# Optimization experiments

Measured on AMD Instinct MI355X. Metric: run time of the kernel, lower is better.

The kernel has to match this reference:

```python
import jax, jax.numpy as jnp
import numpy as np

K = 11            # NATTEN kernel size (hardcoded in module)
HEAD_DIM = 16     # hardcoded: num_heads = attn_dim // 16
SCALE = HEAD_DIM ** -0.5


def _ln(x, g, b, eps=1e-5):
    mu = x.mean(-1, keepdims=True)
    var = jnp.mean((x - mu) ** 2, axis=-1, keepdims=True)
    return (x - mu) * jax.lax.rsqrt(var + eps) * g + b


def _win_idx(L):
    # NATTEN clamped window: start = clip(i - K//2, 0, L-K)
    i = jnp.arange(L)
    start = jnp.clip(i - K // 2, 0, L - K)
    return start[:, None] + jnp.arange(K)[None, :]  # [L, K]


def _neighborhood_attn(q, k, v, rpb):
    # q,k,v: [B, h, H, W, d]; rpb: [h, 2K-1, 2K-1]
    B, h, H, W, d = q.shape
    ii = _win_idx(H)                                  # [H, K]
    jj = _win_idx(W)                                  # [W, K]
    bi = ii - jnp.arange(H)[:, None] + (K - 1)        # rpb row index [H, K]
    bj = jj - jnp.arange(W)[:, None] + (K - 1)        # rpb col index [W, K]
    bias = rpb[:, bi][:, :, :, bj]                    # [h, H, K, W, K]
    k_i = k[:, :, ii]                                 # [B, h, H, K, W, d]
    v_i = v[:, :, ii]
    # QK over the KxK neighborhood; fixed small loop over column offsets
    attn = jnp.stack(
        [jnp.einsum('bhiwd,bhiawd->bhiaw', q, k_i[:, :, :, :, jj[:, c]])
         for c in range(K)], axis=-1)                 # [B, h, H, K, W, K]
    attn = attn + bias[None]
    # reorder neighbors to row-major (ki, kj), softmax over K*K
    attn = attn.transpose(0, 1, 2, 4, 3, 5).reshape(B, h, H, W, K * K)
    attn = jax.nn.softmax(attn, axis=-1).reshape(B, h, H, W, K, K)
    out = jnp.zeros_like(q)
    for c in range(K):
        out = out + jnp.einsum('bhiwa,bhiawd->bhiwd',
                               attn[..., c], v_i[:, :, :, :, jj[:, c]])
    return out  # [B, h, H, W, d]


def setup_inputs() -> dict:
    key = jax.random.key(0)
    ks = jax.random.split(key, 20)
    B, H, W = 16, 64, 64
    HW = H * W
    C = 128       # cost_latent_dim
    VC = 64       # vert_c_dim
    EC = 256      # encoder_latent_dim
    A = 128       # attn_dim
    h = A // HEAD_DIM
    FF = C * 4
    s = 0.02
    inp = {
        'x': jax.random.normal(ks[0], (B, HW, C), jnp.float32),
        'context': jax.random.normal(ks[1], (B, EC, H, W), jnp.float32),
        'ctxn_g': jnp.ones((EC,), jnp.float32),
        'ctxn_b': jnp.zeros((EC,), jnp.float32),
        'ctxp_w': jax.random.normal(ks[2], (EC, VC), jnp.float32) * s,
        'ctxp_b': jnp.zeros((VC,), jnp.float32),
        'n1_g': jnp.ones((C + VC,), jnp.float32),
        'n1_b': jnp.zeros((C + VC,), jnp.float32),
        'n1v_g': jnp.ones((C,), jnp.float32),
        'n1v_b': jnp.zeros((C,), jnp.float32),
        'q_w': jax.random.normal(ks[3], (C + VC, A), jnp.float32) * s,
        'q_b': jnp.zeros((A,), jnp.float32),
        'k_w': jax.random.normal(ks[4], (C + VC, A), jnp.float32) * s,
        'k_b': jnp.zeros((A,), jnp.float32),
        'v_w': jax.random.normal(ks[5], (C, A), jnp.float32) * s,
        'v_b': jnp.zeros((A,), jnp.float32),
        'rpb': jax.random.normal(ks[6], (h, 2 * K - 1, 2 * K - 1), jnp.float32) * s,
        'proj_w': jax.random.normal(ks[7], (A + C, C), jnp.float32) * s,
        'proj_b': jnp.zeros((C,), jnp.float32),
        'n2_g': jnp.ones((C,), jnp.float32),
        'n2_b': jnp.zeros((C,), jnp.float32),
        'f1_w': jax.random.normal(ks[8], (C, FF), jnp.float32) * s,
        'f1_b': jnp.zeros((FF,), jnp.float32),
        'f2_w': jax.random.normal(ks[9], (FF, C), jnp.float32) * s,
        'f2_b': jnp.zeros((C,), jnp.float32),
    }
    return inp


def reference(x, context, ctxn_g, ctxn_b, ctxp_w, ctxp_b, n1_g, n1_b,
              n1v_g, n1v_b, q_w, q_b, k_w, k_b, v_w, v_b, rpb,
              proj_w, proj_b, n2_g, n2_b, f1_w, f1_b, f2_w, f2_b):
    B, HW, C = x.shape
    Bc, Cc, H, W = context.shape
    short_cut = x
    ctx = context.reshape(Bc, Cc, HW).transpose(0, 2, 1)     # [Bc, HW, Cc]
    ctx = _ln(ctx, ctxn_g, ctxn_b) @ ctxp_w + ctxp_b          # [Bc, HW, VC]
    ctx = jnp.tile(ctx, (B // Bc, 1, 1))
    qk = _ln(jnp.concatenate([x, ctx], axis=-1), n1_g, n1_b)
    vv = _ln(x, n1v_g, n1v_b)
    h = q_w.shape[1] // HEAD_DIM
    q = ((qk @ q_w + q_b) * SCALE).reshape(B, H, W, h, HEAD_DIM).transpose(0, 3, 1, 2, 4)
    k = (qk @ k_w + k_b).reshape(B, H, W, h, HEAD_DIM).transpose(0, 3, 1, 2, 4)
    v = (vv @ v_w + v_b).reshape(B, H, W, h, HEAD_DIM).transpose(0, 3, 1, 2, 4)
    o = _neighborhood_attn(q, k, v, rpb)                      # [B, h, H, W, d]
    o = o.transpose(0, 2, 3, 1, 4).reshape(B, HW, -1)
    y = jnp.concatenate([o, short_cut], axis=-1) @ proj_w + proj_b
    y = short_cut + y
    ffn = jax.nn.gelu(_ln(y, n2_g, n2_b) @ f1_w + f1_b, approximate=False) @ f2_w + f2_b
    return y + ffn
```

## Files before the change

kernel.cpp:

```cpp
#include <hip/hip_runtime.h>
#include <hip/hip_bf16.h>
#include <math.h>

typedef __hip_bfloat16 bf16;
typedef float v2f __attribute__((ext_vector_type(2)));
typedef float v4f __attribute__((ext_vector_type(4)));
typedef short v8s __attribute__((ext_vector_type(8)));
typedef _Float16 v2h __attribute__((ext_vector_type(2)));

__device__ __forceinline__ float b2f(bf16 v) { return __bfloat162float(v); }
__device__ __forceinline__ float unpk_lo(unsigned u) { return __uint_as_float(u << 16); }
__device__ __forceinline__ float unpk_hi(unsigned u) { return __uint_as_float(u & 0xffff0000u); }
__device__ __forceinline__ v2f unpk2(unsigned u) {
    v2f r; r.x = __uint_as_float(u << 16); r.y = __uint_as_float(u & 0xffff0000u); return r;
}
__device__ __forceinline__ unsigned pk2(float a, float b) {
    unsigned ua = __float_as_uint(a);
    unsigned ub = __float_as_uint(b);
    ua = (ua + 0x7fffu + ((ua >> 16) & 1u)) >> 16;
    ub = (ub + 0x7fffu + ((ub >> 16) & 1u)) >> 16;
    return ua | (ub << 16);
}
__device__ __forceinline__ short f2bs(float f) {
    unsigned u = __float_as_uint(f);
    u = (u + 0x7fffu + ((u >> 16) & 1u)) >> 16;
    return (short)u;
}
__device__ __forceinline__ v2h u2h(unsigned u) {
    union { unsigned u; v2h h; } c; c.u = u; return c.h;
}
__device__ __forceinline__ float gelu_exact(float x) {
    return 0.5f * x * (1.f + erff(x * 0.70710678118654752440f));
}

#define LOG2E 1.44269504088896340736f

__global__ __launch_bounds__(256) void k_repack(const float* __restrict__ src,
                                                bf16* __restrict__ dst, int K, int N) {
    int idx = blockIdx.x * 256 + threadIdx.x;
    if (idx >= K * N) return;
    int k = idx / N, n = idx % N;
    int kstep = k >> 5, quad = (k & 31) >> 3, j = k & 7;
    int ntile = n >> 4, nn = n & 15;
    size_t di = ((((size_t)kstep * (N >> 4)) + ntile) * 64 + nn + (quad << 4)) * 8 + j;
    dst[di] = __float2bfloat16(src[idx]);
}

__global__ __launch_bounds__(256) void k_repack_g(const float* __restrict__ src,
                                                  const float* __restrict__ g,
                                                  bf16* __restrict__ dst, int K, int N) {
    int idx = blockIdx.x * 256 + threadIdx.x;
    if (idx >= K * N) return;
    int k = idx / N, n = idx % N;
    int kstep = k >> 5, quad = (k & 31) >> 3, j = k & 7;
    int ntile = n >> 4, nn = n & 15;
    size_t di = ((((size_t)kstep * (N >> 4)) + ntile) * 64 + nn + (quad << 4)) * 8 + j;
    dst[di] = __float2bfloat16(src[idx] * g[k]);
}

__global__ __launch_bounds__(256) void k_ctxc(const float* __restrict__ w,
                                              const float* __restrict__ g,
                                              const float* __restrict__ bb,
                                              const float* __restrict__ pb,
                                              float* __restrict__ cgw,
                                              float* __restrict__ cbw) {
    __shared__ float rg_[4][64], rb_[4][64];
    const int n = threadIdx.x & 63, eg = threadIdx.x >> 6;
    float sg = 0.f, sb = 0.f;
    for (int e = eg * 64; e < eg * 64 + 64; ++e) {
        float wv = w[e * 64 + n];
        sg += g[e] * wv;
        sb += bb[e] * wv;
    }
    rg_[eg][n] = sg; rb_[eg][n] = sb;
    __syncthreads();
    if (threadIdx.x < 64) {
        float a = rg_[0][n] + rg_[1][n] + rg_[2][n] + rg_[3][n];
        float c = rb_[0][n] + rb_[1][n] + rb_[2][n] + rb_[3][n];
        cgw[n] = a;
        cbw[n] = c + pb[n];
    }
}

__global__ __launch_bounds__(256) void k_rpb(const float* __restrict__ src,
                                             float* __restrict__ dst, int n) {
    int i = blockIdx.x * 256 + threadIdx.x;
    if (i < n) dst[i] = src[i] * LOG2E - 8.0f;
}

__global__ __launch_bounds__(256) void k_ctx(const float* __restrict__ ctx,
                                             const float* __restrict__ cgw,
                                             const float* __restrict__ cbw,
                                             const bf16* __restrict__ wgf,
                                             bf16* __restrict__ outp) {
    __shared__ short As[32][264];
    __shared__ float redS[8][32];
    __shared__ float redQ[8][32];
    __shared__ float smu[32], srs[32];
    const int t = threadIdx.x;
    const int b = blockIdx.x >> 7;
    const int hw0 = (blockIdx.x & 127) << 5;
    {
        const int r = t & 31, li = t >> 5;
        const float* src = ctx + ((size_t)b * 256 + li * 32) * 4096 + hw0 + r;
        float v[32];
        float s = 0.f, q = 0.f;
#pragma unroll
        for (int j = 0; j < 32; ++j) {
            float x = src[(size_t)j * 4096];
            v[j] = x; s += x; q += x * x;
        }
        redS[li][r] = s;
        redQ[li][r] = q;
        v8s p0, p1, p2, p3;
#pragma unroll
        for (int j = 0; j < 8; ++j) p0[j] = f2bs(v[j]);
#pragma unroll
        for (int j = 0; j < 8; ++j) p1[j] = f2bs(v[8 + j]);
#pragma unroll
        for (int j = 0; j < 8; ++j) p2[j] = f2bs(v[16 + j]);
#pragma unroll
        for (int j = 0; j < 8; ++j) p3[j] = f2bs(v[24 + j]);
        v8s* dst = (v8s*)&As[r][li * 32];
        dst[0] = p0; dst[1] = p1; dst[2] = p2; dst[3] = p3;
    }
    __syncthreads();
    if (t < 32) {
        float s = 0.f, q = 0.f;
#pragma unroll
        for (int k = 0; k < 8; ++k) { s += redS[k][t]; q += redQ[k][t]; }
        float mu = s * (1.f / 256.f);
        float var = q * (1.f / 256.f) - mu * mu;
        smu[t] = mu;
        srs[t] = rsqrtf(var + 1e-5f);
    }
    __syncthreads();
    const int lane = t & 63, wv = t >> 6;
    const int m = lane & 15, quad = lane >> 4;
    v4f acc0 = (v4f){0.f, 0.f, 0.f, 0.f};
    v4f acc1 = (v4f){0.f, 0.f, 0.f, 0.f};
#pragma unroll
    for (int ks = 0; ks < 8; ++ks) {
        v8s a0 = *(const v8s*)&As[m][ks * 32 + quad * 8];
        v8s a1 = *(const v8s*)&As[m + 16][ks * 32 + quad * 8];
        v8s bfr = ((const v8s*)wgf)[((size_t)ks * 4 + wv) * 64 + lane];
        acc0 = __builtin_amdgcn_mfma_f32_16x16x32_bf16(a0, bfr, acc0, 0, 0, 0);
        acc1 = __builtin_amdgcn_mfma_f32_16x16x32_bf16(a1, bfr, acc1, 0, 0, 0);
    }
    const int n = wv * 16 + m;
    const float cg = cgw[n], cb = cbw[n];
    short* obase = (short*)outp + ((size_t)b * 4096 + hw0) * 64 + n;
#pragma unroll
    for (int rg = 0; rg < 4; ++rg) {
        int row = quad * 4 + rg;
        float o = srs[row] * (acc0[rg] - smu[row] * cg) + cb;
        obase[(size_t)row * 64] = f2bs(o);
    }
#pragma unroll
    for (int rg = 0; rg < 4; ++rg) {
        int row = 16 + quad * 4 + rg;
        float o = srs[row] * (acc1[rg] - smu[row] * cg) + cb;
        obase[(size_t)row * 64] = f2bs(o);
    }
}

__global__ __launch_bounds__(256) void k_qkv(const float* __restrict__ x,
                                             const bf16* __restrict__ ctxp,
                                             const float* __restrict__ n1g, const float* __restrict__ n1b,
                                             const float* __restrict__ nvg, const float* __restrict__ nvb,
                                             const bf16* __restrict__ qwf, const float* __restrict__ qb,
                                             const bf16* __restrict__ kwf, const float* __restrict__ kb,
                                             const bf16* __restrict__ vwf, const float* __restrict__ vb,
                                             _Float16* __restrict__ qo, _Float16* __restrict__ ko,
                                             _Float16* __restrict__ vo) {
    __shared__ short Aqk[32][200];
    __shared__ short Av[32][136];
    const int t = threadIdx.x;
    const size_t row0 = (size_t)blockIdx.x * 32;
    {
        const int r = t >> 3, li = t & 7;
        const float* xr = x + (row0 + r) * 128 + li * 16;
        float v[16];
        float sx1 = 0.f, sx2 = 0.f;
#pragma unroll
        for (int k4 = 0; k4 < 4; ++k4) {
            float4 vv = *(const float4*)(xr + 4 * k4);
            v[4 * k4 + 0] = vv.x; v[4 * k4 + 1] = vv.y; v[4 * k4 + 2] = vv.z; v[4 * k4 + 3] = vv.w;
            sx1 += vv.x + vv.y + vv.z + vv.w;
            sx2 += vv.x * vv.x + vv.y * vv.y + vv.z * vv.z + vv.w * vv.w;
        }
        float cv[8];
        float sc1 = 0.f, sc2 = 0.f;
        {
            uint4 cu = *(const uint4*)(ctxp + (row0 + r) * 64 + li * 8);
            v2f p0 = unpk2(cu.x), p1 = unpk2(cu.y), p2 = unpk2(cu.z), p3 = unpk2(cu.w);
            cv[0] = p0.x; cv[1] = p0.y; cv[2] = p1.x; cv[3] = p1.y;
            cv[4] = p2.x; cv[5] = p2.y; cv[6] = p3.x; cv[7] = p3.y;
#pragma unroll
            for (int k = 0; k < 8; ++k) { sc1 += cv[k]; sc2 += cv[k] * cv[k]; }
        }
#pragma unroll
        for (int o = 1; o < 8; o <<= 1) {
            sx1 += __shfl_xor(sx1, o); sx2 += __shfl_xor(sx2, o);
            sc1 += __shfl_xor(sc1, o); sc2 += __shfl_xor(sc2, o);
        }
        float mu  = (sx1 + sc1) * (1.f / 192.f);
        float rs  = rsqrtf((sx2 + sc2) * (1.f / 192.f) - mu * mu + 1e-5f);
        float muv = sx1 * (1.f / 128.f);
        float rsv = rsqrtf(sx2 * (1.f / 128.f) - muv * muv + 1e-5f);
        v8s q0, q1, vv0, vv1, cc;
#pragma unroll
        for (int k = 0; k < 8; ++k) {
            int c = li * 16 + k;
            q0[k]  = f2bs((v[k] - mu) * rs * n1g[c] + n1b[c]);
            vv0[k] = f2bs((v[k] - muv) * rsv * nvg[c] + nvb[c]);
        }
#pragma unroll
        for (int k = 0; k < 8; ++k) {
            int c = li * 16 + 8 + k;
            q1[k]  = f2bs((v[8 + k] - mu) * rs * n1g[c] + n1b[c]);
            vv1[k] = f2bs((v[8 + k] - muv) * rsv * nvg[c] + nvb[c]);
        }
#pragma unroll
        for (int k = 0; k < 8; ++k) {
            int c = 128 + li * 8 + k;
            cc[k] = f2bs((cv[k] - mu) * rs * n1g[c] + n1b[c]);
        }
        *(v8s*)&Aqk[r][li * 16]     = q0;
        *(v8s*)&Aqk[r][li * 16 + 8] = q1;
        *(v8s*)&Aqk[r][128 + li * 8] = cc;
        *(v8s*)&Av[r][li * 16]     = vv0;
        *(v8s*)&Av[r][li * 16 + 8] = vv1;
    }
    __syncthreads();
    const int lane = t & 63, wv = t >> 6;
    const int m = lane & 15, quad = lane >> 4;
    const int ntb = wv * 2;
    v4f aq[2][2], ak[2][2], av[2][2];
#pragma unroll
    for (int a = 0; a < 2; ++a)
#pragma unroll
        for (int b = 0; b < 2; ++b) {
            aq[a][b] = (v4f){0.f, 0.f, 0.f, 0.f};
            ak[a][b] = (v4f){0.f, 0.f, 0.f, 0.f};
            av[a][b] = (v4f){0.f, 0.f, 0.f, 0.f};
        }
#pragma unroll
    for (int ks = 0; ks < 6; ++ks) {
        v8s a0 = *(const v8s*)&Aqk[m][ks * 32 + quad * 8];
        v8s a1 = *(const v8s*)&Aqk[m + 16][ks * 32 + quad * 8];
        const v8s* bpq = (const v8s*)qwf + ((size_t)ks * 8 + ntb) * 64 + lane;
        const v8s* bpk = (const v8s*)kwf + ((size_t)ks * 8 + ntb) * 64 + lane;
#pragma unroll
        for (int nt = 0; nt < 2; ++nt) {
            v8s bq = bpq[nt * 64];
            v8s bk = bpk[nt * 64];
            aq[0][nt] = __builtin_amdgcn_mfma_f32_16x16x32_bf16(a0, bq, aq[0][nt], 0, 0, 0);
            aq[1][nt] = __builtin_amdgcn_mfma_f32_16x16x32_bf16(a1, bq, aq[1][nt], 0, 0, 0);
            ak[0][nt] = __builtin_amdgcn_mfma_f32_16x16x32_bf16(a0, bk, ak[0][nt], 0, 0, 0);
            ak[1][nt] = __builtin_amdgcn_mfma_f32_16x16x32_bf16(a1, bk, ak[1][nt], 0, 0, 0);
        }
    }
#pragma unroll
    for (int ks = 0; ks < 4; ++ks) {
        v8s a0 = *(const v8s*)&Av[m][ks * 32 + quad * 8];
        v8s a1 = *(const v8s*)&Av[m + 16][ks * 32 + quad * 8];
        const v8s* bpv = (const v8s*)vwf + ((size_t)ks * 8 + ntb) * 64 + lane;
#pragma unroll
        for (int nt = 0; nt < 2; ++nt) {
            v8s bv = bpv[nt * 64];
            av[0][nt] = __builtin_amdgcn_mfma_f32_16x16x32_bf16(a0, bv, av[0][nt], 0, 0, 0);
            av[1][nt] = __builtin_amdgcn_mfma_f32_16x16x32_bf16(a1, bv, av[1][nt], 0, 0, 0);
        }
    }
#pragma unroll
    for (int nt = 0; nt < 2; ++nt) {
        int n = (ntb + nt) * 16 + m;
        int head = n >> 4, d = n & 15;
        float qbv = qb[n], kbv = kb[n], vbv = vb[n];
#pragma unroll
        for (int mt = 0; mt < 2; ++mt)
#pragma unroll
            for (int rg = 0; rg < 4; ++rg) {
                int rowg = (int)row0 + mt * 16 + quad * 4 + rg;
                int b = rowg >> 12, hw = rowg & 4095;
                size_t oi = (((size_t)b * 8 + head) * 4096 + hw) * 16 + d;
                qo[oi] = (_Float16)((aq[mt][nt][rg] + qbv) * (0.25f * LOG2E));
                ko[oi] = (_Float16)(ak[mt][nt][rg] + kbv);
                vo[oi] = (_Float16)(av[mt][nt][rg] + vbv);
            }
    }
}

__global__ __launch_bounds__(256) void k_attn(const _Float16* __restrict__ qws,
                                              const _Float16* __restrict__ kws,
                                              const _Float16* __restrict__ vws,
                                              const float* __restrict__ rpbl2,
                                              bf16* __restrict__ ows) {
    __shared__ unsigned ktv[14][64][20];
    const int tid  = threadIdx.x;
    const int bh   = blockIdx.x >> 4;
    const int i0   = (blockIdx.x & 15) << 2;
    const int head = bh & 7;
    int start_min = i0 - 5; if (start_min < 0) start_min = 0; if (start_min > 53) start_min = 53;
    const unsigned* ku = (const unsigned*)kws;
    const unsigned* vu = (const unsigned*)vws;
    const size_t gbase = ((size_t)bh * 4096 + (size_t)start_min * 64) * 8;
    for (int idx = tid; idx < 1792; idx += 256) {
        int a = idx >> 7, rem = idx & 127, col = rem >> 1, h4 = (rem & 1) * 4;
        if (start_min + a < 64) {
            *(uint4*)&ktv[a][col][h4]     = *(const uint4*)(ku + gbase + (size_t)a * 512 + col * 8 + h4);
            *(uint4*)&ktv[a][col][8 + h4] = *(const uint4*)(vu + gbase + (size_t)a * 512 + col * 8 + h4);
        }
    }
    __syncthreads();
    const int wv = tid >> 6;
    const int j  = tid & 63;
    const int i  = i0 + wv;
    int start_i = i - 5; if (start_i < 0) start_i = 0; if (start_i > 53) start_i = 53;
    const int off = start_i - start_min;
    v2h qh[8];
    {
        const uint4* qp = (const uint4*)(qws + ((size_t)bh * 4096 + i * 64 + j) * 16);
        uint4 q0 = qp[0], q1 = qp[1];
        qh[0] = u2h(q0.x); qh[1] = u2h(q0.y); qh[2] = u2h(q0.z); qh[3] = u2h(q0.w);
        qh[4] = u2h(q1.x); qh[5] = u2h(q1.y); qh[6] = u2h(q1.z); qh[7] = u2h(q1.w);
    }
    int start_j = j - 5; if (start_j < 0) start_j = 0; if (start_j > 53) start_j = 53;
    float l = 0.f;
    v2h acc[8];
#pragma unroll
    for (int d = 0; d < 8; ++d) acc[d] = (v2h){(_Float16)0.f, (_Float16)0.f};
    const float* rpb_h = rpbl2 + head * 441 + (start_j - j + 10);
    for (int a = 0; a < 11; ++a) {
        const int r = off + a;
        const float* rb = rpb_h + (start_i + a - i + 10) * 21;
#pragma unroll
        for (int c = 0; c < 11; ++c) {
            const unsigned* cp = ktv[r][start_j + c];
            uint4 k0 = *(const uint4*)(cp);
            uint4 k1 = *(const uint4*)(cp + 4);
            uint4 v0 = *(const uint4*)(cp + 8);
            uint4 v1 = *(const uint4*)(cp + 12);
            float sa = __builtin_amdgcn_fdot2(qh[0], u2h(k0.x), rb[c], false);
            sa = __builtin_amdgcn_fdot2(qh[1], u2h(k0.y), sa, false);
            sa = __builtin_amdgcn_fdot2(qh[2], u2h(k0.z), sa, false);
            sa = __builtin_amdgcn_fdot2(qh[3], u2h(k0.w), sa, false);
            float sb = __builtin_amdgcn_fdot2(qh[4], u2h(k1.x), 0.f, false);
            sb = __builtin_amdgcn_fdot2(qh[5], u2h(k1.y), sb, false);
            sb = __builtin_amdgcn_fdot2(qh[6], u2h(k1.z), sb, false);
            sb = __builtin_amdgcn_fdot2(qh[7], u2h(k1.w), sb, false);
            float p = __builtin_amdgcn_exp2f(sa + sb);
            l += p;
            _Float16 ph = (_Float16)p;
            v2h p2 = {ph, ph};
            acc[0] += u2h(v0.x) * p2;
            acc[1] += u2h(v0.y) * p2;
            acc[2] += u2h(v0.z) * p2;
            acc[3] += u2h(v0.w) * p2;
            acc[4] += u2h(v1.x) * p2;
            acc[5] += u2h(v1.y) * p2;
            acc[6] += u2h(v1.z) * p2;
            acc[7] += u2h(v1.w) * p2;
        }
    }
    float inv = 1.f / l;
    int b = bh >> 3;
    unsigned* op = (unsigned*)ows + ((size_t)b * 4096 + i * 64 + j) * 64 + head * 8;
#pragma unroll
    for (int d2 = 0; d2 < 8; ++d2)
        op[d2] = pk2((float)acc[d2].x * inv, (float)acc[d2].y * inv);
}

__global__ __launch_bounds__(256) void k_proj(const float* __restrict__ x,
                                              const bf16* __restrict__ ows,
                                              const bf16* __restrict__ pwf,
                                              const float* __restrict__ pb,
                                              float* __restrict__ yws) {
    __shared__ short An[32][264];
    const int t = threadIdx.x;
    const size_t row0 = (size_t)blockIdx.x * 32;
    {
        const int r = t >> 3, li = t & 7;
        const uint4* osrc = (const uint4*)(ows + (row0 + r) * 128 + li * 16);
        uint4 o0 = osrc[0], o1 = osrc[1];
        *(uint4*)&An[r][li * 16]     = o0;
        *(uint4*)&An[r][li * 16 + 8] = o1;
        const float* xr = x + (row0 + r) * 128 + li * 16;
        v8s xa, xb;
#pragma unroll
        for (int k4 = 0; k4 < 2; ++k4) {
            float4 vv = *(const float4*)(xr + 4 * k4);
            xa[4 * k4 + 0] = f2bs(vv.x); xa[4 * k4 + 1] = f2bs(vv.y);
            xa[4 * k4 + 2] = f2bs(vv.z); xa[4 * k4 + 3] = f2bs(vv.w);
        }
#pragma unroll
        for (int k4 = 0; k4 < 2; ++k4) {
            float4 vv = *(const float4*)(xr + 8 + 4 * k4);
            xb[4 * k4 + 0] = f2bs(vv.x); xb[4 * k4 + 1] = f2bs(vv.y);
            xb[4 * k4 + 2] = f2bs(vv.z); xb[4 * k4 + 3] = f2bs(vv.w);
        }
        *(v8s*)&An[r][128 + li * 16]     = xa;
        *(v8s*)&An[r][128 + li * 16 + 8] = xb;
    }
    __syncthreads();
    const int lane = t & 63, wv = t >> 6;
    const int m = lane & 15, quad = lane >> 4;
    const int ntb = wv * 2;
    v4f acc[2][2];
#pragma unroll
    for (int a = 0; a < 2; ++a)
#pragma unroll
        for (int b = 0; b < 2; ++b) acc[a][b] = (v4f){0.f, 0.f, 0.f, 0.f};
#pragma unroll
    for (int ks = 0; ks < 8; ++ks) {
        v8s a0 = *(const v8s*)&An[m][ks * 32 + quad * 8];
        v8s a1 = *(const v8s*)&An[m + 16][ks * 32 + quad * 8];
        const v8s* bp = (const v8s*)pwf + ((size_t)ks * 8 + ntb) * 64 + lane;
#pragma unroll
        for (int nt = 0; nt < 2; ++nt) {
            v8s b = bp[nt * 64];
            acc[0][nt] = __builtin_amdgcn_mfma_f32_16x16x32_bf16(a0, b, acc[0][nt], 0, 0, 0);
            acc[1][nt] = __builtin_amdgcn_mfma_f32_16x16x32_bf16(a1, b, acc[1][nt], 0, 0, 0);
        }
    }
#pragma unroll
    for (int nt = 0; nt < 2; ++nt) {
        int n = (ntb + nt) * 16 + m;
        float bv = pb[n];
#pragma unroll
        for (int mt = 0; mt < 2; ++mt)
#pragma unroll
            for (int rg = 0; rg < 4; ++rg) {
                int row = mt * 16 + quad * 4 + rg;
                size_t gi = (row0 + row) * 128 + n;
                yws[gi] = x[gi] + bv + acc[mt][nt][rg];
            }
    }
}

__global__ __launch_bounds__(256) void k_ffn(const float* __restrict__ yws,
                                             const float* __restrict__ g, const float* __restrict__ bb,
                                             const bf16* __restrict__ w1f, const float* __restrict__ b1,
                                             const bf16* __restrict__ w2f, const float* __restrict__ b2,
                                             float* __restrict__ outp) {
    __shared__ short An[32][136];
    __shared__ short Hs[32][520];
    const int t = threadIdx.x;
    const size_t row0 = (size_t)blockIdx.x * 32;
    {
        const int r = t >> 3, li = t & 7;
        const float* yr = yws + (row0 + r) * 128 + li * 16;
        float v[16];
        float s1 = 0.f, s2 = 0.f;
#pragma unroll
        for (int k4 = 0; k4 < 4; ++k4) {
            float4 vv = *(const float4*)(yr + 4 * k4);
            v[4 * k4 + 0] = vv.x; v[4 * k4 + 1] = vv.y; v[4 * k4 + 2] = vv.z; v[4 * k4 + 3] = vv.w;
            s1 += vv.x + vv.y + vv.z + vv.w;
            s2 += vv.x * vv.x + vv.y * vv.y + vv.z * vv.z + vv.w * vv.w;
        }
#pragma unroll
        for (int o = 1; o < 8; o <<= 1) { s1 += __shfl_xor(s1, o); s2 += __shfl_xor(s2, o); }
        float mu = s1 * (1.f / 128.f);
        float rs = rsqrtf(s2 * (1.f / 128.f) - mu * mu + 1e-5f);
        v8s lo, hi;
#pragma unroll
        for (int k = 0; k < 8; ++k) {
            int c = li * 16 + k;
            lo[k] = f2bs((v[k] - mu) * rs * g[c] + bb[c]);
        }
#pragma unroll
        for (int k = 0; k < 8; ++k) {
            int c = li * 16 + 8 + k;
            hi[k] = f2bs((v[8 + k] - mu) * rs * g[c] + bb[c]);
        }
        *(v8s*)&An[r][li * 16]     = lo;
        *(v8s*)&An[r][li * 16 + 8] = hi;
    }
    __syncthreads();
    const int lane = t & 63, wv = t >> 6;
    const int m = lane & 15, quad = lane >> 4;
    v4f acc1[2][8];
#pragma unroll
    for (int a = 0; a < 2; ++a)
#pragma unroll
        for (int b = 0; b < 8; ++b) acc1[a][b] = (v4f){0.f, 0.f, 0.f, 0.f};
    const int n0w = wv * 128;
#pragma unroll
    for (int ks = 0; ks < 4; ++ks) {
        v8s a0 = *(const v8s*)&An[m][ks * 32 + quad * 8];
        v8s a1 = *(const v8s*)&An[m + 16][ks * 32 + quad * 8];
        const v8s* bp = (const v8s*)w1f + ((size_t)ks * 32 + (n0w >> 4)) * 64 + lane;
#pragma unroll
        for (int nt = 0; nt < 8; ++nt) {
            v8s b = bp[nt * 64];
            acc1[0][nt] = __builtin_amdgcn_mfma_f32_16x16x32_bf16(a0, b, acc1[0][nt], 0, 0, 0);
            acc1[1][nt] = __builtin_amdgcn_mfma_f32_16x16x32_bf16(a1, b, acc1[1][nt], 0, 0, 0);
        }
    }
#pragma unroll
    for (int nt = 0; nt < 8; ++nt) {
        int n = n0w + nt * 16 + m;
        float b1v = b1[n];
#pragma unroll
        for (int mt = 0; mt < 2; ++mt)
#pragma unroll
            for (int rg = 0; rg < 4; ++rg)
                Hs[mt * 16 + quad * 4 + rg][n] = f2bs(gelu_exact(acc1[mt][nt][rg] + b1v));
    }
    __syncthreads();
    v4f acc2[2][2];
#pragma unroll
    for (int a = 0; a < 2; ++a)
#pragma unroll
        for (int b = 0; b < 2; ++b) acc2[a][b] = (v4f){0.f, 0.f, 0.f, 0.f};
    const int ntb = wv * 2;
#pragma unroll
    for (int ks = 0; ks < 16; ++ks) {
        v8s a0 = *(const v8s*)&Hs[m][ks * 32 + quad * 8];
        v8s a1 = *(const v8s*)&Hs[m + 16][ks * 32 + quad * 8];
        const v8s* bp = (const v8s*)w2f + ((size_t)ks * 8 + ntb) * 64 + lane;
#pragma unroll
        for (int nt = 0; nt < 2; ++nt) {
            v8s b = bp[nt * 64];
            acc2[0][nt] = __builtin_amdgcn_mfma_f32_16x16x32_bf16(a0, b, acc2[0][nt], 0, 0, 0);
            acc2[1][nt] = __builtin_amdgcn_mfma_f32_16x16x32_bf16(a1, b, acc2[1][nt], 0, 0, 0);
        }
    }
#pragma unroll
    for (int nt = 0; nt < 2; ++nt) {
        int n = (ntb + nt) * 16 + m;
        float b2v = b2[n];
#pragma unroll
        for (int mt = 0; mt < 2; ++mt)
#pragma unroll
            for (int rg = 0; rg < 4; ++rg) {
                int row = mt * 16 + quad * 4 + rg;
                size_t gi = (row0 + row) * 128 + n;
                outp[gi] = yws[gi] + b2v + acc2[mt][nt][rg];
            }
    }
}

extern "C" void kernel_launch(void* const* d_in, const int* in_sizes, int n_in,
                              void* d_out, int out_size, void* d_ws, size_t ws_size,
                              hipStream_t stream) {
    const float* x      = (const float*)d_in[0];
    const float* ctx    = (const float*)d_in[1];
    const float* ctxn_g = (const float*)d_in[2];
    const float* ctxn_b = (const float*)d_in[3];
    const float* ctxp_w = (const float*)d_in[4];
    const float* ctxp_b = (const float*)d_in[5];
    const float* n1_g   = (const float*)d_in[6];
    const float* n1_b   = (const float*)d_in[7];
    const float* n1v_g  = (const float*)d_in[8];
    const float* n1v_b  = (const float*)d_in[9];
    const float* q_w    = (const float*)d_in[10];
    const float* q_b    = (const float*)d_in[11];
    const float* k_w    = (const float*)d_in[12];
    const float* k_b    = (const float*)d_in[13];
    const float* v_w    = (const float*)d_in[14];
    const float* v_b    = (const float*)d_in[15];
    const float* rpb    = (const float*)d_in[16];
    const float* proj_w = (const float*)d_in[17];
    const float* proj_b = (const float*)d_in[18];
    const float* n2_g   = (const float*)d_in[19];
    const float* n2_b   = (const float*)d_in[20];
    const float* f1_w   = (const float*)d_in[21];
    const float* f1_b   = (const float*)d_in[22];
    const float* f2_w   = (const float*)d_in[23];
    const float* f2_b   = (const float*)d_in[24];
    float* out = (float*)d_out;

    char* ws = (char*)d_ws;
    bf16*      ctxp = (bf16*)(ws);
    _Float16*  qws  = (_Float16*)(ws + 8388608);
    _Float16*  kws  = (_Float16*)(ws + 25165824);
    _Float16*  vws  = (_Float16*)(ws + 41943040);
    bf16*      ows  = (bf16*)(ws + 58720256);
    float*     yws  = (float*)(ws + 8388608);
    char* frag = ws + 75497472;
    bf16*  w1f  = (bf16*)(frag);
    bf16*  w2f  = (bf16*)(frag + 131072);
    bf16*  qwf  = (bf16*)(frag + 262144);
    bf16*  kwf  = (bf16*)(frag + 311296);
    bf16*  vwf  = (bf16*)(frag + 360448);
    bf16*  pwf  = (bf16*)(frag + 393216);
    float* rpl2 = (float*)(frag + 458752);
    bf16*  wgf  = (bf16*)(ws + 8388608);
    float* cgw  = (float*)(ws + 8388608 + 32768);
    float* cbw  = (float*)(ws + 8388608 + 33024);

    k_repack<<<256, 256, 0, stream>>>(f1_w, w1f, 128, 512);
    k_repack<<<256, 256, 0, stream>>>(f2_w, w2f, 512, 128);
    k_repack<<<96,  256, 0, stream>>>(q_w,  qwf, 192, 128);
    k_repack<<<96,  256, 0, stream>>>(k_w,  kwf, 192, 128);
    k_repack<<<64,  256, 0, stream>>>(v_w,  vwf, 128, 128);
    k_repack<<<128, 256, 0, stream>>>(proj_w, pwf, 256, 128);
    k_repack_g<<<64, 256, 0, stream>>>(ctxp_w, ctxn_g, wgf, 256, 64);
    k_ctxc<<<1, 256, 0, stream>>>(ctxp_w, ctxn_g, ctxn_b, ctxp_b, cgw, cbw);
    k_rpb<<<14, 256, 0, stream>>>(rpb, rpl2, 8 * 441);
    k_ctx<<<2048, 256, 0, stream>>>(ctx, cgw, cbw, wgf, ctxp);
    k_qkv<<<2048, 256, 0, stream>>>(x, ctxp, n1_g, n1_b, n1v_g, n1v_b,
                                    qwf, q_b, kwf, k_b, vwf, v_b, qws, kws, vws);
    k_attn<<<2048, 256, 0, stream>>>(qws, kws, vws, rpl2, ows);
    k_proj<<<2048, 256, 0, stream>>>(x, ows, pwf, proj_b, yws);
    k_ffn<<<2048, 256, 0, stream>>>(yws, n2_g, n2_b, w1f, f1_b, w2f, f2_b, out);
}
```

Before: 379.6 us.

## Register-block neighborhood attention over four query rows sharing K/V LDS reads

Each thread now computes four consecutive query rows and iterates over the union of their row windows. Each K/V vector loaded from shared memory is reused across the four queries, with a large negative penalty masking positions outside a given row's window. Shared memory is relaid out column-major with padding and sized to cover 8 query rows per 128-thread block. This cuts LDS read traffic per output, in exchange for extra masked dot products and exps, larger LDS per block and lower occupancy.

```diff
diff --git a/kernel.cpp b/kernel.cpp
--- a/kernel.cpp
+++ b/kernel.cpp
@@ -292,84 +292,104 @@
     }
 }
 
-__global__ __launch_bounds__(256) void k_attn(const _Float16* __restrict__ qws,
+__global__ __launch_bounds__(128) void k_attn(const _Float16* __restrict__ qws,
                                               const _Float16* __restrict__ kws,
                                               const _Float16* __restrict__ vws,
                                               const float* __restrict__ rpbl2,
                                               bf16* __restrict__ ows) {
-    __shared__ unsigned ktv[14][64][20];
+    __shared__ unsigned ktv[64 * 292];
     const int tid  = threadIdx.x;
-    const int bh   = blockIdx.x >> 4;
-    const int i0   = (blockIdx.x & 15) << 2;
+    const int bh   = blockIdx.x >> 3;
+    const int i0   = (blockIdx.x & 7) << 3;
     const int head = bh & 7;
-    int start_min = i0 - 5; if (start_min < 0) start_min = 0; if (start_min > 53) start_min = 53;
+    int start_min = i0 - 5; if (start_min < 0) start_min = 0; if (start_min > 46) start_min = 46;
     const unsigned* ku = (const unsigned*)kws;
     const unsigned* vu = (const unsigned*)vws;
-    const size_t gbase = ((size_t)bh * 4096 + (size_t)start_min * 64) * 8;
-    for (int idx = tid; idx < 1792; idx += 256) {
-        int a = idx >> 7, rem = idx & 127, col = rem >> 1, h4 = (rem & 1) * 4;
-        if (start_min + a < 64) {
-            *(uint4*)&ktv[a][col][h4]     = *(const uint4*)(ku + gbase + (size_t)a * 512 + col * 8 + h4);
-            *(uint4*)&ktv[a][col][8 + h4] = *(const uint4*)(vu + gbase + (size_t)a * 512 + col * 8 + h4);
-        }
+    const size_t gK = ((size_t)bh * 4096 + (size_t)start_min * 64) * 8;
+    for (int idx = tid; idx < 4608; idx += 128) {
+        int col = idx & 63, slot = (idx >> 6) & 3, row = idx >> 8;
+        const unsigned* src = (slot < 2 ? ku : vu) + gK + (size_t)row * 512 + col * 8 + (slot & 1) * 4;
+        *(uint4*)&ktv[col * 292 + row * 16 + slot * 4] = *(const uint4*)src;
     }
     __syncthreads();
     const int wv = tid >> 6;
     const int j  = tid & 63;
-    const int i  = i0 + wv;
-    int start_i = i - 5; if (start_i < 0) start_i = 0; if (start_i > 53) start_i = 53;
-    const int off = start_i - start_min;
-    v2h qh[8];
-    {
-        const uint4* qp = (const uint4*)(qws + ((size_t)bh * 4096 + i * 64 + j) * 16);
+    const int ib = i0 + 4 * wv;
+    int start_j = j - 5; if (start_j < 0) start_j = 0; if (start_j > 53) start_j = 53;
+    v2h qh[4][8];
+#pragma unroll
+    for (int q = 0; q < 4; ++q) {
+        const uint4* qp = (const uint4*)(qws + ((size_t)bh * 4096 + (ib + q) * 64 + j) * 16);
         uint4 q0 = qp[0], q1 = qp[1];
-        qh[0] = u2h(q0.x); qh[1] = u2h(q0.y); qh[2] = u2h(q0.z); qh[3] = u2h(q0.w);
-        qh[4] = u2h(q1.x); qh[5] = u2h(q1.y); qh[6] = u2h(q1.z); qh[7] = u2h(q1.w);
-    }
-    int start_j = j - 5; if (start_j < 0) start_j = 0; if (start_j > 53) start_j = 53;
-    float l = 0.f;
-    v2h acc[8];
-#pragma unroll
-    for (int d = 0; d < 8; ++d) acc[d] = (v2h){(_Float16)0.f, (_Float16)0.f};
-    const float* rpb_h = rpbl2 + head * 441 + (start_j - j + 10);
-    for (int a = 0; a < 11; ++a) {
-        const int r = off + a;
-        const float* rb = rpb_h + (start_i + a - i + 10) * 21;
+        qh[q][0] = u2h(q0.x); qh[q][1] = u2h(q0.y); qh[q][2] = u2h(q0.z); qh[q][3] = u2h(q0.w);
+        qh[q][4] = u2h(q1.x); qh[q][5] = u2h(q1.y); qh[q][6] = u2h(q1.z); qh[q][7] = u2h(q1.w);
+    }
+    int st0 = ib - 5; if (st0 < 0) st0 = 0; if (st0 > 53) st0 = 53;
+    int st3 = ib - 2; if (st3 < 0) st3 = 0; if (st3 > 53) st3 = 53;
+    const int nr = st3 - st0 + 11;
+    float l[4] = {0.f, 0.f, 0.f, 0.f};
+    v2h acc[4][8];
+#pragma unroll
+    for (int q = 0; q < 4; ++q)
+#pragma unroll
+        for (int d = 0; d < 8; ++d) acc[q][d] = (v2h){(_Float16)0.f, (_Float16)0.f};
+    const float* rpb_base = rpbl2 + head * 441 + (start_j - j + 10);
+    const int lds_base = start_j * 292;
+    for (int au = 0; au < nr; ++au) {
+        const int a_abs = st0 + au;
+        const int r16 = (a_abs - start_min) * 16;
+        const float* rb[4];
+        float pen[4];
+#pragma unroll
+        for (int q = 0; q < 4; ++q) {
+            int iq = ib + q;
+            int sq = iq - 5; if (sq < 0) sq = 0; if (sq > 53) sq = 53;
+            int ri = a_abs - iq + 10;
+            int ric = ri < 0 ? 0 : (ri > 20 ? 20 : ri);
+            rb[q] = rpb_base + ric * 21;
+            pen[q] = ((unsigned)(a_abs - sq) <= 10u) ? 0.f : -30000.f;
+        }
 #pragma unroll
         for (int c = 0; c < 11; ++c) {
-            const unsigned* cp = ktv[r][start_j + c];
+            const unsigned* cp = &ktv[lds_base + c * 292 + r16];
             uint4 k0 = *(const uint4*)(cp);
             uint4 k1 = *(const uint4*)(cp + 4);
             uint4 v0 = *(const uint4*)(cp + 8);
             uint4 v1 = *(const uint4*)(cp + 12);
-            float sa = __builtin_amdgcn_fdot2(qh[0], u2h(k0.x), rb[c], false);
-            sa = __builtin_amdgcn_fdot2(qh[1], u2h(k0.y), sa, false);
-            sa = __builtin_amdgcn_fdot2(qh[2], u2h(k0.z), sa, false);
-            sa = __builtin_amdgcn_fdot2(qh[3], u2h(k0.w), sa, false);
-            float sb = __builtin_amdgcn_fdot2(qh[4], u2h(k1.x), 0.f, false);
-            sb = __builtin_amdgcn_fdot2(qh[5], u2h(k1.y), sb, false);
-            sb = __builtin_amdgcn_fdot2(qh[6], u2h(k1.z), sb, false);
-            sb = __builtin_amdgcn_fdot2(qh[7], u2h(k1.w), sb, false);
-            float p = __builtin_amdgcn_exp2f(sa + sb);
-            l += p;
-            _Float16 ph = (_Float16)p;
-            v2h p2 = {ph, ph};
-            acc[0] += u2h(v0.x) * p2;
-            acc[1] += u2h(v0.y) * p2;
-            acc[2] += u2h(v0.z) * p2;
-            acc[3] += u2h(v0.w) * p2;
-            acc[4] += u2h(v1.x) * p2;
-            acc[5] += u2h(v1.y) * p2;
-            acc[6] += u2h(v1.z) * p2;
-            acc[7] += u2h(v1.w) * p2;
-        }
-    }
-    float inv = 1.f / l;
-    int b = bh >> 3;
-    unsigned* op = (unsigned*)ows + ((size_t)b * 4096 + i * 64 + j) * 64 + head * 8;
-#pragma unroll
-    for (int d2 = 0; d2 < 8; ++d2)
-        op[d2] = pk2((float)acc[d2].x * inv, (float)acc[d2].y * inv);
+#pragma unroll
+            for (int q = 0; q < 4; ++q) {
+                float sa = __builtin_amdgcn_fdot2(qh[q][0], u2h(k0.x), rb[q][c] + pen[q], false);
+                sa = __builtin_amdgcn_fdot2(qh[q][1], u2h(k0.y), sa, false);
+                sa = __builtin_amdgcn_fdot2(qh[q][2], u2h(k0.z), sa, false);
+                sa = __builtin_amdgcn_fdot2(qh[q][3], u2h(k0.w), sa, false);
+                float sb = __builtin_amdgcn_fdot2(qh[q][4], u2h(k1.x), 0.f, false);
+                sb = __builtin_amdgcn_fdot2(qh[q][5], u2h(k1.y), sb, false);
+                sb = __builtin_amdgcn_fdot2(qh[q][6], u2h(k1.z), sb, false);
+                sb = __builtin_amdgcn_fdot2(qh[q][7], u2h(k1.w), sb, false);
+                float p = __builtin_amdgcn_exp2f(sa + sb);
+                l[q] += p;
+                _Float16 ph = (_Float16)p;
+                v2h p2 = {ph, ph};
+                acc[q][0] += u2h(v0.x) * p2;
+                acc[q][1] += u2h(v0.y) * p2;
+                acc[q][2] += u2h(v0.z) * p2;
+                acc[q][3] += u2h(v0.w) * p2;
+                acc[q][4] += u2h(v1.x) * p2;
+                acc[q][5] += u2h(v1.y) * p2;
+                acc[q][6] += u2h(v1.z) * p2;
+                acc[q][7] += u2h(v1.w) * p2;
+            }
+        }
+    }
+    const int b = bh >> 3;
+#pragma unroll
+    for (int q = 0; q < 4; ++q) {
+        float inv = 1.f / l[q];
+        unsigned* op = (unsigned*)ows + ((size_t)b * 4096 + (ib + q) * 64 + j) * 64 + head * 8;
+#pragma unroll
+        for (int d2 = 0; d2 < 8; ++d2)
+            op[d2] = pk2((float)acc[q][d2].x * inv, (float)acc[q][d2].y * inv);
+    }
 }
 
 __global__ __launch_bounds__(256) void k_proj(const float* __restrict__ x,
@@ -604,7 +624,7 @@
     k_ctx<<<2048, 256, 0, stream>>>(ctx, cgw, cbw, wgf, ctxp);
     k_qkv<<<2048, 256, 0, stream>>>(x, ctxp, n1_g, n1_b, n1v_g, n1v_b,
                                     qwf, q_b, kwf, k_b, vwf, v_b, qws, kws, vws);
-    k_attn<<<2048, 256, 0, stream>>>(qws, kws, vws, rpl2, ows);
+    k_attn<<<1024, 128, 0, stream>>>(qws, kws, vws, rpl2, ows);
     k_proj<<<2048, 256, 0, stream>>>(x, ows, pwf, proj_b, yws);
     k_ffn<<<2048, 256, 0, stream>>>(yws, n2_g, n2_b, w1f, f1_b, w2f, f2_b, out);
 }
```

Measured after the change: 421.4 us. 1.11x slower.

## Fuse projection with FFN and coalesce QKV stores via LDS transpose

Applied to the files above, without the earlier changes.

Merges the projection and FFN kernels into one, so the residual y stays in shared memory rather than making a float32 round trip through global memory and needing an extra launch. Shared memory is aliased across stages, with added barriers, to keep the LDS footprint bounded. The QKV kernel now stages its fp16 outputs in LDS and writes them as 16-byte per-head rows instead of scattered 2-byte stores. The cost is more barriers and higher LDS use per block, which may lower occupancy.

```diff
diff --git a/kernel.cpp b/kernel.cpp
--- a/kernel.cpp
+++ b/kernel.cpp
@@ -25,6 +25,9 @@
     unsigned u = __float_as_uint(f);
     u = (u + 0x7fffu + ((u >> 16) & 1u)) >> 16;
     return (short)u;
+}
+__device__ __forceinline__ short f2hs(float f) {
+    union { _Float16 h; short s; } c; c.h = (_Float16)f; return c.s;
 }
 __device__ __forceinline__ v2h u2h(unsigned u) {
     union { unsigned u; v2h h; } c; c.u = u; return c.h;
@@ -173,8 +176,9 @@
                                              const bf16* __restrict__ vwf, const float* __restrict__ vb,
                                              _Float16* __restrict__ qo, _Float16* __restrict__ ko,
                                              _Float16* __restrict__ vo) {
-    __shared__ short Aqk[32][200];
-    __shared__ short Av[32][136];
+    __shared__ short SM[13056];
+    short* Aqk = SM;
+    short* Av  = SM + 6400;
     const int t = threadIdx.x;
     const size_t row0 = (size_t)blockIdx.x * 32;
     {
@@ -226,11 +230,11 @@
             int c = 128 + li * 8 + k;
             cc[k] = f2bs((cv[k] - mu) * rs * n1g[c] + n1b[c]);
         }
-        *(v8s*)&Aqk[r][li * 16]     = q0;
-        *(v8s*)&Aqk[r][li * 16 + 8] = q1;
-        *(v8s*)&Aqk[r][128 + li * 8] = cc;
-        *(v8s*)&Av[r][li * 16]     = vv0;
-        *(v8s*)&Av[r][li * 16 + 8] = vv1;
+        *(v8s*)&Aqk[r * 200 + li * 16]      = q0;
+        *(v8s*)&Aqk[r * 200 + li * 16 + 8]  = q1;
+        *(v8s*)&Aqk[r * 200 + 128 + li * 8] = cc;
+        *(v8s*)&Av[r * 136 + li * 16]       = vv0;
+        *(v8s*)&Av[r * 136 + li * 16 + 8]   = vv1;
     }
     __syncthreads();
     const int lane = t & 63, wv = t >> 6;
@@ -247,8 +251,8 @@
         }
 #pragma unroll
     for (int ks = 0; ks < 6; ++ks) {
-        v8s a0 = *(const v8s*)&Aqk[m][ks * 32 + quad * 8];
-        v8s a1 = *(const v8s*)&Aqk[m + 16][ks * 32 + quad * 8];
+        v8s a0 = *(const v8s*)&Aqk[m * 200 + ks * 32 + quad * 8];
+        v8s a1 = *(const v8s*)&Aqk[(m + 16) * 200 + ks * 32 + quad * 8];
         const v8s* bpq = (const v8s*)qwf + ((size_t)ks * 8 + ntb) * 64 + lane;
         const v8s* bpk = (const v8s*)kwf + ((size_t)ks * 8 + ntb) * 64 + lane;
 #pragma unroll
@@ -263,8 +267,8 @@
     }
 #pragma unroll
     for (int ks = 0; ks < 4; ++ks) {
-        v8s a0 = *(const v8s*)&Av[m][ks * 32 + quad * 8];
-        v8s a1 = *(const v8s*)&Av[m + 16][ks * 32 + quad * 8];
+        v8s a0 = *(const v8s*)&Av[m * 136 + ks * 32 + quad * 8];
+        v8s a1 = *(const v8s*)&Av[(m + 16) * 136 + ks * 32 + quad * 8];
         const v8s* bpv = (const v8s*)vwf + ((size_t)ks * 8 + ntb) * 64 + lane;
 #pragma unroll
         for (int nt = 0; nt < 2; ++nt) {
@@ -273,22 +277,36 @@
             av[1][nt] = __builtin_amdgcn_mfma_f32_16x16x32_bf16(a1, bv, av[1][nt], 0, 0, 0);
         }
     }
+    __syncthreads();
+    short* Tq = SM;
+    short* Tk = SM + 4352;
+    short* Tv = SM + 8704;
 #pragma unroll
     for (int nt = 0; nt < 2; ++nt) {
         int n = (ntb + nt) * 16 + m;
-        int head = n >> 4, d = n & 15;
         float qbv = qb[n], kbv = kb[n], vbv = vb[n];
 #pragma unroll
         for (int mt = 0; mt < 2; ++mt)
 #pragma unroll
             for (int rg = 0; rg < 4; ++rg) {
-                int rowg = (int)row0 + mt * 16 + quad * 4 + rg;
-                int b = rowg >> 12, hw = rowg & 4095;
-                size_t oi = (((size_t)b * 8 + head) * 4096 + hw) * 16 + d;
-                qo[oi] = (_Float16)((aq[mt][nt][rg] + qbv) * (0.25f * LOG2E));
-                ko[oi] = (_Float16)(ak[mt][nt][rg] + kbv);
-                vo[oi] = (_Float16)(av[mt][nt][rg] + vbv);
+                int row = mt * 16 + quad * 4 + rg;
+                Tq[row * 136 + n] = f2hs((aq[mt][nt][rg] + qbv) * (0.25f * LOG2E));
+                Tk[row * 136 + n] = f2hs(ak[mt][nt][rg] + kbv);
+                Tv[row * 136 + n] = f2hs(av[mt][nt][rg] + vbv);
             }
+    }
+    __syncthreads();
+    {
+        const int h = t >> 5, w = t & 31;
+        const size_t qrow = row0 + w;
+        const int bq = (int)(qrow >> 12), hw = (int)(qrow & 4095);
+        const size_t ob = (((size_t)bq * 8 + h) * 4096 + hw) * 16;
+        *(uint4*)(qo + ob)     = *(const uint4*)&Tq[w * 136 + h * 16];
+        *(uint4*)(qo + ob + 8) = *(const uint4*)&Tq[w * 136 + h * 16 + 8];
+        *(uint4*)(ko + ob)     = *(const uint4*)&Tk[w * 136 + h * 16];
+        *(uint4*)(ko + ob + 8) = *(const uint4*)&Tk[w * 136 + h * 16 + 8];
+        *(uint4*)(vo + ob)     = *(const uint4*)&Tv[w * 136 + h * 16];
+        *(uint4*)(vo + ob + 8) = *(const uint4*)&Tv[w * 136 + h * 16 + 8];
     }
 }
 
@@ -372,93 +390,91 @@
         op[d2] = pk2((float)acc[d2].x * inv, (float)acc[d2].y * inv);
 }
 
-__global__ __launch_bounds__(256) void k_proj(const float* __restrict__ x,
-                                              const bf16* __restrict__ ows,
-                                              const bf16* __restrict__ pwf,
-                                              const float* __restrict__ pb,
-                                              float* __restrict__ yws) {
-    __shared__ short An[32][264];
+__global__ __launch_bounds__(256) void k_pf(const float* __restrict__ x,
+                                            const bf16* __restrict__ ows,
+                                            const bf16* __restrict__ pwf,
+                                            const float* __restrict__ pb,
+                                            const float* __restrict__ g, const float* __restrict__ bb,
+                                            const bf16* __restrict__ w1f, const float* __restrict__ b1,
+                                            const bf16* __restrict__ w2f, const float* __restrict__ b2,
+                                            float* __restrict__ outp) {
+    __shared__ short RA[16896];
+    __shared__ float Ys[32 * 132];
+    short* An = RA;
+    float* Xs = (float*)(RA + 8448);
     const int t = threadIdx.x;
     const size_t row0 = (size_t)blockIdx.x * 32;
     {
         const int r = t >> 3, li = t & 7;
         const uint4* osrc = (const uint4*)(ows + (row0 + r) * 128 + li * 16);
         uint4 o0 = osrc[0], o1 = osrc[1];
-        *(uint4*)&An[r][li * 16]     = o0;
-        *(uint4*)&An[r][li * 16 + 8] = o1;
+        *(uint4*)&An[r * 264 + li * 16]     = o0;
+        *(uint4*)&An[r * 264 + li * 16 + 8] = o1;
         const float* xr = x + (row0 + r) * 128 + li * 16;
         v8s xa, xb;
 #pragma unroll
         for (int k4 = 0; k4 < 2; ++k4) {
             float4 vv = *(const float4*)(xr + 4 * k4);
+            *(float4*)&Xs[r * 132 + li * 16 + 4 * k4] = vv;
             xa[4 * k4 + 0] = f2bs(vv.x); xa[4 * k4 + 1] = f2bs(vv.y);
             xa[4 * k4 + 2] = f2bs(vv.z); xa[4 * k4 + 3] = f2bs(vv.w);
         }
 #pragma unroll
         for (int k4 = 0; k4 < 2; ++k4) {
             float4 vv = *(const float4*)(xr + 8 + 4 * k4);
+            *(float4*)&Xs[r * 132 + li * 16 + 8 + 4 * k4] = vv;
             xb[4 * k4 + 0] = f2bs(vv.x); xb[4 * k4 + 1] = f2bs(vv.y);
             xb[4 * k4 + 2] = f2bs(vv.z); xb[4 * k4 + 3] = f2bs(vv.w);
         }
-        *(v8s*)&An[r][128 + li * 16]     = xa;
-        *(v8s*)&An[r][128 + li * 16 + 8] = xb;
+        *(v8s*)&An[r * 264 + 128 + li * 16]     = xa;
+        *(v8s*)&An[r * 264 + 128 + li * 16 + 8] = xb;
     }
     __syncthreads();
     const int lane = t & 63, wv = t >> 6;
     const int m = lane & 15, quad = lane >> 4;
     const int ntb = wv * 2;
-    v4f acc[2][2];
-#pragma unroll
-    for (int a = 0; a < 2; ++a)
-#pragma unroll
-        for (int b = 0; b < 2; ++b) acc[a][b] = (v4f){0.f, 0.f, 0.f, 0.f};
-#pragma unroll
-    for (int ks = 0; ks < 8; ++ks) {
-        v8s a0 = *(const v8s*)&An[m][ks * 32 + quad * 8];
-        v8s a1 = *(const v8s*)&An[m + 16][ks * 32 + quad * 8];
-        const v8s* bp = (const v8s*)pwf + ((size_t)ks * 8 + ntb) * 64 + lane;
+    {
+        v4f acc[2][2];
+#pragma unroll
+        for (int a = 0; a < 2; ++a)
+#pragma unroll
+            for (int b = 0; b < 2; ++b) acc[a][b] = (v4f){0.f, 0.f, 0.f, 0.f};
+#pragma unroll
+        for (int ks = 0; ks < 8; ++ks) {
+            v8s a0 = *(const v8s*)&An[m * 264 + ks * 32 + quad * 8];
+            v8s a1 = *(const v8s*)&An[(m + 16) * 264 + ks * 32 + quad * 8];
+            const v8s* bp = (const v8s*)pwf + ((size_t)ks * 8 + ntb) * 64 + lane;
+#pragma unroll
+            for (int nt = 0; nt < 2; ++nt) {
+                v8s b = bp[nt * 64];
+                acc[0][nt] = __builtin_amdgcn_mfma_f32_16x16x32_bf16(a0, b, acc[0][nt], 0, 0, 0);
+                acc[1][nt] = __builtin_amdgcn_mfma_f32_16x16x32_bf16(a1, b, acc[1][nt], 0, 0, 0);
+            }
+        }
 #pragma unroll
         for (int nt = 0; nt < 2; ++nt) {
-            v8s b = bp[nt * 64];
-            acc[0][nt] = __builtin_amdgcn_mfma_f32_16x16x32_bf16(a0, b, acc[0][nt], 0, 0, 0);
-            acc[1][nt] = __builtin_amdgcn_mfma_f32_16x16x32_bf16(a1, b, acc[1][nt], 0, 0, 0);
-        }
-    }
-#pragma unroll
-    for (int nt = 0; nt < 2; ++nt) {
-        int n = (ntb + nt) * 16 + m;
-        float bv = pb[n];
-#pragma unroll
-        for (int mt = 0; mt < 2; ++mt)
-#pragma unroll
-            for (int rg = 0; rg < 4; ++rg) {
-                int row = mt * 16 + quad * 4 + rg;
-                size_t gi = (row0 + row) * 128 + n;
-                yws[gi] = x[gi] + bv + acc[mt][nt][rg];
-            }
-    }
-}
-
-__global__ __launch_bounds__(256) void k_ffn(const float* __restrict__ yws,
-                                             const float* __restrict__ g, const float* __restrict__ bb,
-                                             const bf16* __restrict__ w1f, const float* __restrict__ b1,
-                                             const bf16* __restrict__ w2f, const float* __restrict__ b2,
-                                             float* __restrict__ outp) {
-    __shared__ short An[32][136];
-    __shared__ short Hs[32][520];
-    const int t = threadIdx.x;
-    const size_t row0 = (size_t)blockIdx.x * 32;
+            int n = (ntb + nt) * 16 + m;
+            float bv = pb[n];
+#pragma unroll
+            for (int mt = 0; mt < 2; ++mt)
+#pragma unroll
+                for (int rg = 0; rg < 4; ++rg) {
+                    int row = mt * 16 + quad * 4 + rg;
+                    Ys[row * 132 + n] = Xs[row * 132 + n] + bv + acc[mt][nt][rg];
+                }
+        }
+    }
+    __syncthreads();
+    short* An2 = RA;
     {
         const int r = t >> 3, li = t & 7;
-        const float* yr = yws + (row0 + r) * 128 + li * 16;
+        const float* yr = &Ys[r * 132 + li * 16];
         float v[16];
         float s1 = 0.f, s2 = 0.f;
 #pragma unroll
-        for (int k4 = 0; k4 < 4; ++k4) {
-            float4 vv = *(const float4*)(yr + 4 * k4);
-            v[4 * k4 + 0] = vv.x; v[4 * k4 + 1] = vv.y; v[4 * k4 + 2] = vv.z; v[4 * k4 + 3] = vv.w;
-            s1 += vv.x + vv.y + vv.z + vv.w;
-            s2 += vv.x * vv.x + vv.y * vv.y + vv.z * vv.z + vv.w * vv.w;
+        for (int k = 0; k < 16; ++k) {
+            float vv = yr[k];
+            v[k] = vv; s1 += vv; s2 += vv * vv;
         }
 #pragma unroll
         for (int o = 1; o < 8; o <<= 1) { s1 += __shfl_xor(s1, o); s2 += __shfl_xor(s2, o); }
@@ -475,12 +491,10 @@
             int c = li * 16 + 8 + k;
             hi[k] = f2bs((v[8 + k] - mu) * rs * g[c] + bb[c]);
         }
-        *(v8s*)&An[r][li * 16]     = lo;
-        *(v8s*)&An[r][li * 16 + 8] = hi;
-    }
-    __syncthreads();
-    const int lane = t & 63, wv = t >> 6;
-    const int m = lane & 15, quad = lane >> 4;
+        *(v8s*)&An2[r * 136 + li * 16]     = lo;
+        *(v8s*)&An2[r * 136 + li * 16 + 8] = hi;
+    }
+    __syncthreads();
     v4f acc1[2][8];
 #pragma unroll
     for (int a = 0; a < 2; ++a)
@@ -489,8 +503,8 @@
     const int n0w = wv * 128;
 #pragma unroll
     for (int ks = 0; ks < 4; ++ks) {
-        v8s a0 = *(const v8s*)&An[m][ks * 32 + quad * 8];
-        v8s a1 = *(const v8s*)&An[m + 16][ks * 32 + quad * 8];
+        v8s a0 = *(const v8s*)&An2[m * 136 + ks * 32 + quad * 8];
+        v8s a1 = *(const v8s*)&An2[(m + 16) * 136 + ks * 32 + quad * 8];
         const v8s* bp = (const v8s*)w1f + ((size_t)ks * 32 + (n0w >> 4)) * 64 + lane;
 #pragma unroll
         for (int nt = 0; nt < 8; ++nt) {
@@ -499,6 +513,8 @@
             acc1[1][nt] = __builtin_amdgcn_mfma_f32_16x16x32_bf16(a1, b, acc1[1][nt], 0, 0, 0);
         }
     }
+    __syncthreads();
+    short* Hs = RA;
 #pragma unroll
     for (int nt = 0; nt < 8; ++nt) {
         int n = n0w + nt * 16 + m;
@@ -507,7 +523,7 @@
         for (int mt = 0; mt < 2; ++mt)
 #pragma unroll
             for (int rg = 0; rg < 4; ++rg)
-                Hs[mt * 16 + quad * 4 + rg][n] = f2bs(gelu_exact(acc1[mt][nt][rg] + b1v));
+                Hs[(mt * 16 + quad * 4 + rg) * 520 + n] = f2bs(gelu_exact(acc1[mt][nt][rg] + b1v));
     }
     __syncthreads();
     v4f acc2[2][2];
@@ -515,11 +531,10 @@
     for (int a = 0; a < 2; ++a)
 #pragma unroll
         for (int b = 0; b < 2; ++b) acc2[a][b] = (v4f){0.f, 0.f, 0.f, 0.f};
-    const int ntb = wv * 2;
 #pragma unroll
     for (int ks = 0; ks < 16; ++ks) {
-        v8s a0 = *(const v8s*)&Hs[m][ks * 32 + quad * 8];
-        v8s a1 = *(const v8s*)&Hs[m + 16][ks * 32 + quad * 8];
+        v8s a0 = *(const v8s*)&Hs[m * 520 + ks * 32 + quad * 8];
+        v8s a1 = *(const v8s*)&Hs[(m + 16) * 520 + ks * 32 + quad * 8];
         const v8s* bp = (const v8s*)w2f + ((size_t)ks * 8 + ntb) * 64 + lane;
 #pragma unroll
         for (int nt = 0; nt < 2; ++nt) {
@@ -538,7 +553,7 @@
             for (int rg = 0; rg < 4; ++rg) {
                 int row = mt * 16 + quad * 4 + rg;
                 size_t gi = (row0 + row) * 128 + n;
-                outp[gi] = yws[gi] + b2v + acc2[mt][nt][rg];
+                outp[gi] = Ys[row * 132 + n] + b2v + acc2[mt][nt][rg];
             }
     }
 }
@@ -579,7 +594,6 @@
     _Float16*  kws  = (_Float16*)(ws + 25165824);
     _Float16*  vws  = (_Float16*)(ws + 41943040);
     bf16*      ows  = (bf16*)(ws + 58720256);
-    float*     yws  = (float*)(ws + 8388608);
     char* frag = ws + 75497472;
     bf16*  w1f  = (bf16*)(frag);
     bf16*  w2f  = (bf16*)(frag + 131072);
@@ -605,6 +619,6 @@
     k_qkv<<<2048, 256, 0, stream>>>(x, ctxp, n1_g, n1_b, n1v_g, n1v_b,
                                     qwf, q_b, kwf, k_b, vwf, v_b, qws, kws, vws);
     k_attn<<<2048, 256, 0, stream>>>(qws, kws, vws, rpl2, ows);
-    k_proj<<<2048, 256, 0, stream>>>(x, ows, pwf, proj_b, yws);
-    k_ffn<<<2048, 256, 0, stream>>>(yws, n2_g, n2_b, w1f, f1_b, w2f, f2_b, out);
-}
+    k_pf<<<2048, 256, 0, stream>>>(x, ows, pwf, proj_b, n2_g, n2_b,
+                                   w1f, f1_b, w2f, f2_b, out);
+}
```

New measurement: 374.6 us. Within noise of the previous version (-1.3%).
